# Performance work log

Measured on AMD Instinct MI355X. Metric: run time of the kernel, lower is better.

## Reference

```python
import jax, jax.numpy as jnp
import numpy as np

B = 2            # batch size
N_PRE = 50000    # presynaptic neurons
N_POST = 50000   # postsynaptic neurons
N_SYN = 10_000_000   # synapses (avg in-degree 200)
N_TYPES = 20     # synapse/receptor types (rows of basis table)
N_BASIS = 5      # receptor basis functions
SPIKE_P = 0.02   # spike probability per neuron per step


def setup_inputs() -> dict:
    key = jax.random.key(0)
    k1, k2, k3, k4, k5 = jax.random.split(key, 5)
    # binary spike buffer, like rec_z_buf (values in {0,1})
    rec_z_buf = (jax.random.uniform(k1, (B, N_PRE)) < SPIKE_P).astype(jnp.float32)
    weight_values = jax.random.normal(k2, (N_SYN,), dtype=jnp.float32) * 0.1
    synaptic_basis_weights = jax.random.uniform(k3, (N_TYPES, N_BASIS), dtype=jnp.float32)
    # col 0 = postsynaptic index, col 1 = presynaptic index
    synapse_indices = jax.random.randint(k4, (N_SYN, 2), 0, N_POST, dtype=jnp.int32)
    syn_ids = jax.random.randint(k5, (N_SYN,), 0, N_TYPES, dtype=jnp.int32)
    return {
        'rec_z_buf': rec_z_buf,
        'weight_values': weight_values,
        'synaptic_basis_weights': synaptic_basis_weights,
        'synapse_indices': synapse_indices,
        'syn_ids': syn_ids,
        'n_post': N_POST,
    }


def reference(rec_z_buf, weight_values, synaptic_basis_weights, synapse_indices, syn_ids, n_post):
    """I[b, post, r] = sum_syn spike[b, pre_syn] * W_syn * basis[syn_id_syn, r].

    Equivalent to the TF custom op: since spikes are binary, gating by
    spike > 0 equals multiplying by the spike value.
    Returns flat [B * n_post, n_basis] like i_rec_flat.
    """
    post = synapse_indices[:, 0]            # [n_syn]
    pre = synapse_indices[:, 1]             # [n_syn]
    # per-synapse weighted basis contribution [n_syn, R]
    contrib = weight_values[:, None] * synaptic_basis_weights[syn_ids]
    gathered = rec_z_buf[:, pre]            # [B, n_syn] spike gate per synapse
    per_syn = gathered[:, :, None] * contrib[None, :, :]   # [B, n_syn, R]
    # scatter-add into postsynaptic neurons, per batch element
    i_rec = jax.vmap(lambda x: jax.ops.segment_sum(x, post, num_segments=n_post))(per_syn)
    return i_rec.reshape(-1, i_rec.shape[-1])   # [B * n_post, R]
```

## Files before the change

### kernel.cpp

```cpp
#include <hip/hip_runtime.h>

#define N_PRE_C   50000
#define N_TYPES_C 20
#define N_BASIS_C 5
#define NB        2
#define WORDS32   1568

typedef unsigned long long ull;
typedef unsigned int uint_t;

__global__ __launch_bounds__(256) void pack_spikes(const float* __restrict__ rec_z,
                                                   uint_t* __restrict__ mask32,
                                                   float4* __restrict__ zbuf,
                                                   int zquads) {
    const int b = blockIdx.y;
    const int i = blockIdx.x * 256 + threadIdx.x;
    float v = 0.f;
    if (i < N_PRE_C) v = rec_z[b * N_PRE_C + i];
    const ull m = __ballot(v > 0.f);
    if ((threadIdx.x & 63) == 0) {
        const int w32 = i >> 5;
        mask32[(w32 + 0) * NB + b] = (uint_t)(m & 0xffffffffull);
        mask32[(w32 + 1) * NB + b] = (uint_t)(m >> 32);
    }

    if (zbuf != nullptr) {
        const int nt = gridDim.x * gridDim.y * 256;
        int q = (blockIdx.y * gridDim.x + blockIdx.x) * 256 + threadIdx.x;
        const float4 z = make_float4(0.f, 0.f, 0.f, 0.f);
        for (; q < zquads; q += nt) zbuf[q] = z;
    }
}

__global__ __launch_bounds__(256) void syn_scatter_t(
    const int4*  __restrict__ idx2,
    const float4* __restrict__ w4,
    const int4*  __restrict__ sid4,
    const uint2* __restrict__ mask2,
    float* __restrict__ out_t,
    int n_post, int n_syn) {
    __shared__ __align__(16) uint2 sm[WORDS32];
    {
        const uint4* msrc = (const uint4*)mask2;
        uint4* mdst = (uint4*)sm;
        for (int t = threadIdx.x; t < WORDS32 / 2; t += 256) mdst[t] = msrc[t];
    }
    __syncthreads();

    const int t = blockIdx.x * 256 + threadIdx.x;
    const long base = (long)t * 4;
    if (base >= n_syn) return;
    const int np20 = n_post * N_TYPES_C;

    if (base + 4 <= n_syn) {
        const int4 p01 = idx2[t * 2];
        const int4 p23 = idx2[t * 2 + 1];
        const uint2 m0 = sm[p01.y >> 5];
        const uint2 m1 = sm[p01.w >> 5];
        const uint2 m2 = sm[p23.y >> 5];
        const uint2 m3 = sm[p23.w >> 5];
        const uint_t b0 = 1u << (p01.y & 31);
        const uint_t b1 = 1u << (p01.w & 31);
        const uint_t b2 = 1u << (p23.y & 31);
        const uint_t b3 = 1u << (p23.w & 31);
        const uint_t f0 = (m0.x | m0.y) & b0;
        const uint_t f1 = (m1.x | m1.y) & b1;
        const uint_t f2 = (m2.x | m2.y) & b2;
        const uint_t f3 = (m3.x | m3.y) & b3;
        if (f0 | f1 | f2 | f3) {
            const float4 wv = w4[t];
            const int4   sv = sid4[t];
            if (f0) {
                const int o = p01.x * N_TYPES_C + sv.x;
                if (m0.x & b0) unsafeAtomicAdd(out_t + o, wv.x);
                if (m0.y & b0) unsafeAtomicAdd(out_t + o + np20, wv.x);
            }
            if (f1) {
                const int o = p01.z * N_TYPES_C + sv.y;
                if (m1.x & b1) unsafeAtomicAdd(out_t + o, wv.y);
                if (m1.y & b1) unsafeAtomicAdd(out_t + o + np20, wv.y);
            }
            if (f2) {
                const int o = p23.x * N_TYPES_C + sv.z;
                if (m2.x & b2) unsafeAtomicAdd(out_t + o, wv.z);
                if (m2.y & b2) unsafeAtomicAdd(out_t + o + np20, wv.z);
            }
            if (f3) {
                const int o = p23.z * N_TYPES_C + sv.w;
                if (m3.x & b3) unsafeAtomicAdd(out_t + o, wv.w);
                if (m3.y & b3) unsafeAtomicAdd(out_t + o + np20, wv.w);
            }
        }
    } else {
        const int*   idx = (const int*)idx2;
        const float* w   = (const float*)w4;
        const int*   sid = (const int*)sid4;
        for (long s = base; s < n_syn; ++s) {
            const int post = idx[2 * s], pre = idx[2 * s + 1];
            const uint2 mw = sm[pre >> 5];
            const uint_t bit = 1u << (pre & 31);
            if (((mw.x | mw.y) & bit) == 0u) continue;
            const int o = post * N_TYPES_C + sid[s];
            if (mw.x & bit) unsafeAtomicAdd(out_t + o, w[s]);
            if (mw.y & bit) unsafeAtomicAdd(out_t + o + np20, w[s]);
        }
    }
}

__global__ __launch_bounds__(256) void combine_basis(
    const float* __restrict__ out_t,
    const float* __restrict__ basis,
    float* __restrict__ out, int rows) {
    __shared__ float sb[N_TYPES_C * N_BASIS_C];
    if (threadIdx.x < N_TYPES_C * N_BASIS_C) sb[threadIdx.x] = basis[threadIdx.x];
    __syncthreads();

    const int r = blockIdx.x * 256 + threadIdx.x;
    if (r >= rows) return;
    const float4* p = (const float4*)(out_t + (long)r * N_TYPES_C);
    float4 v0 = p[0], v1 = p[1], v2 = p[2], v3 = p[3], v4 = p[4];
    float vt[N_TYPES_C] = {v0.x, v0.y, v0.z, v0.w, v1.x, v1.y, v1.z, v1.w,
                           v2.x, v2.y, v2.z, v2.w, v3.x, v3.y, v3.z, v3.w,
                           v4.x, v4.y, v4.z, v4.w};
    float acc[N_BASIS_C] = {0.f, 0.f, 0.f, 0.f, 0.f};
    #pragma unroll
    for (int t = 0; t < N_TYPES_C; ++t) {
        #pragma unroll
        for (int k = 0; k < N_BASIS_C; ++k)
            acc[k] += vt[t] * sb[t * N_BASIS_C + k];
    }
    float* o = out + (long)r * N_BASIS_C;
    #pragma unroll
    for (int k = 0; k < N_BASIS_C; ++k) o[k] = acc[k];
}

__global__ __launch_bounds__(256) void syn_scatter_direct(
    const int4* __restrict__ idx2, const float4* __restrict__ w4,
    const int4* __restrict__ sid4, const float* __restrict__ basis,
    const uint2* __restrict__ mask2, float* __restrict__ out,
    int n_post, int n_syn) {
    __shared__ __align__(16) uint2 sm[WORDS32];
    __shared__ float sb[N_TYPES_C][N_BASIS_C];
    for (int t = threadIdx.x; t < WORDS32; t += 256) sm[t] = mask2[t];
    for (int t = threadIdx.x; t < N_TYPES_C * N_BASIS_C; t += 256)
        ((float*)sb)[t] = basis[t];
    __syncthreads();
    const int t = blockIdx.x * 256 + threadIdx.x;
    const long base = (long)t * 4;
    if (base >= n_syn) return;

    auto apply = [&](int post, int pre, float wv, int tt) {
        const uint2 mw = sm[pre >> 5];
        const uint_t bit = 1u << (pre & 31);
        if (((mw.x | mw.y) & bit) == 0u) return;
        const float* bs = sb[tt];
        float c[N_BASIS_C];
        #pragma unroll
        for (int k = 0; k < N_BASIS_C; ++k) c[k] = wv * bs[k];
        if (mw.x & bit) {
            float* o = out + (long)post * N_BASIS_C;
            #pragma unroll
            for (int k = 0; k < N_BASIS_C; ++k) unsafeAtomicAdd(o + k, c[k]);
        }
        if (mw.y & bit) {
            float* o = out + (long)(n_post + post) * N_BASIS_C;
            #pragma unroll
            for (int k = 0; k < N_BASIS_C; ++k) unsafeAtomicAdd(o + k, c[k]);
        }
    };

    if (base + 4 <= n_syn) {
        const int4   p01 = idx2[t * 2];
        const int4   p23 = idx2[t * 2 + 1];
        const float4 wv  = w4[t];
        const int4   sv  = sid4[t];
        apply(p01.x, p01.y, wv.x, sv.x);
        apply(p01.z, p01.w, wv.y, sv.y);
        apply(p23.x, p23.y, wv.z, sv.z);
        apply(p23.z, p23.w, wv.w, sv.w);
    } else {
        const int*   idx = (const int*)idx2;
        const float* w   = (const float*)w4;
        const int*   sid = (const int*)sid4;
        for (long s = base; s < n_syn; ++s)
            apply(idx[2 * s], idx[2 * s + 1], w[s], sid[s]);
    }
}

extern "C" void kernel_launch(void* const* d_in, const int* in_sizes, int n_in,
                              void* d_out, int out_size, void* d_ws, size_t ws_size,
                              hipStream_t stream) {
    const float* rec_z   = (const float*)d_in[0];
    const float* weights = (const float*)d_in[1];
    const float* basis   = (const float*)d_in[2];
    const int*   synidx  = (const int*)d_in[3];
    const int*   synids  = (const int*)d_in[4];
    float*       out     = (float*)d_out;

    const int n_syn  = in_sizes[4];
    const int rows   = out_size / N_BASIS_C;
    const int n_post = rows / NB;
    const int n_thr  = (n_syn + 3) / 4;
    const int blocks = (n_thr + 255) / 256;

    const size_t out_t_bytes = (size_t)rows * N_TYPES_C * sizeof(float);
    const size_t mask_bytes  = (size_t)WORDS32 * NB * sizeof(uint_t);

    if (ws_size >= out_t_bytes + mask_bytes) {
        float*  out_t  = (float*)d_ws;
        uint_t* mask32 = (uint_t*)((char*)d_ws + out_t_bytes);

        const int zquads = (int)(out_t_bytes / sizeof(float4));
        pack_spikes<<<dim3(WORDS32 * 32 / 256, NB), 256, 0, stream>>>(
            rec_z, mask32, (float4*)out_t, zquads);

        syn_scatter_t<<<blocks, 256, 0, stream>>>(
            (const int4*)synidx, (const float4*)weights, (const int4*)synids,
            (const uint2*)mask32, out_t, n_post, n_syn);

        combine_basis<<<(rows + 255) / 256, 256, 0, stream>>>(out_t, basis, out, rows);
    } else {
        uint_t* mask32 = (uint_t*)d_ws;
        hipMemsetAsync(d_out, 0, (size_t)out_size * sizeof(float), stream);
        pack_spikes<<<dim3(WORDS32 * 32 / 256, NB), 256, 0, stream>>>(
            rec_z, mask32, nullptr, 0);
        syn_scatter_direct<<<blocks, 256, 0, stream>>>(
            (const int4*)synidx, (const float4*)weights, (const int4*)synids,
            basis, (const uint2*)mask32, out, n_post, n_syn);
    }
}
```

Before: 198.7 us.

## Fuse pack, scatter and basis combine into one cooperative persistent kernel

Replaces the three-kernel sequence (spike packing plus zeroing, synapse scatter, basis combine) with a single cooperative kernel that uses grid-wide syncs between phases and grid-stride loops sized to the occupancy limit, capped at 2048 blocks. It aims to remove kernel launch gaps and inter-kernel drain and tail overhead. In exchange it adds two grid barriers with fences, and far fewer resident threads to hide the latency of the gathers and atomics. It falls back to the old path if the cooperative launch fails.

```diff
diff --git a/kernel.cpp b/kernel.cpp
--- a/kernel.cpp
+++ b/kernel.cpp
@@ -1,13 +1,147 @@
 #include <hip/hip_runtime.h>
+#include <hip/hip_cooperative_groups.h>
+
+namespace cg = cooperative_groups;
 
 #define N_PRE_C   50000
 #define N_TYPES_C 20
 #define N_BASIS_C 5
 #define NB        2
 #define WORDS32   1568
+#define PACK_LANES (NB * WORDS32 * 32)
 
 typedef unsigned long long ull;
 typedef unsigned int uint_t;
+
+__global__ __launch_bounds__(256) void fused_all(
+    const float* __restrict__ rec_z,
+    const float4* __restrict__ w4,
+    const float* __restrict__ basis,
+    const int4*  __restrict__ idx2,
+    const int4*  __restrict__ sid4,
+    uint_t* __restrict__ mask32,
+    float*  __restrict__ out_t,
+    float*  __restrict__ out,
+    int n_post, int n_syn, int rows) {
+    __shared__ __align__(16) uint2 sm[WORDS32];
+    __shared__ float sb[N_TYPES_C * N_BASIS_C];
+
+    const int tid = threadIdx.x;
+    const int gid = blockIdx.x * 256 + tid;
+    const int nthreads = gridDim.x * 256;
+
+    if (tid < N_TYPES_C * N_BASIS_C) sb[tid] = basis[tid];
+
+    if (gid < PACK_LANES) {
+        const int b = gid / (WORDS32 * 32);
+        const int i = gid % (WORDS32 * 32);
+        float v = 0.f;
+        if (i < N_PRE_C) v = rec_z[b * N_PRE_C + i];
+        const ull m = __ballot(v > 0.f);
+        if ((tid & 63) == 0) {
+            const int w32 = i >> 5;
+            mask32[(w32 + 0) * NB + b] = (uint_t)(m & 0xffffffffull);
+            mask32[(w32 + 1) * NB + b] = (uint_t)(m >> 32);
+        }
+    }
+    {
+        const int zq = rows * N_TYPES_C / 4;
+        float4* zp = (float4*)out_t;
+        const float4 z = make_float4(0.f, 0.f, 0.f, 0.f);
+        for (int q = gid; q < zq; q += nthreads) zp[q] = z;
+    }
+
+    __threadfence();
+    cg::this_grid().sync();
+    __threadfence();
+
+    {
+        const uint4* msrc = (const uint4*)mask32;
+        uint4* mdst = (uint4*)sm;
+        for (int t = tid; t < WORDS32 / 2; t += 256) mdst[t] = msrc[t];
+    }
+    __syncthreads();
+
+    const int np20 = n_post * N_TYPES_C;
+    const int nq = n_syn >> 2;
+    for (int t = gid; t < nq; t += nthreads) {
+        const int4 p01 = idx2[(long)t * 2];
+        const int4 p23 = idx2[(long)t * 2 + 1];
+        const uint2 m0 = sm[p01.y >> 5];
+        const uint2 m1 = sm[p01.w >> 5];
+        const uint2 m2 = sm[p23.y >> 5];
+        const uint2 m3 = sm[p23.w >> 5];
+        const uint_t b0 = 1u << (p01.y & 31);
+        const uint_t b1 = 1u << (p01.w & 31);
+        const uint_t b2 = 1u << (p23.y & 31);
+        const uint_t b3 = 1u << (p23.w & 31);
+        const uint_t f0 = (m0.x | m0.y) & b0;
+        const uint_t f1 = (m1.x | m1.y) & b1;
+        const uint_t f2 = (m2.x | m2.y) & b2;
+        const uint_t f3 = (m3.x | m3.y) & b3;
+        if (f0 | f1 | f2 | f3) {
+            const float4 wv = w4[t];
+            const int4   sv = sid4[t];
+            if (f0) {
+                const int o = p01.x * N_TYPES_C + sv.x;
+                if (m0.x & b0) unsafeAtomicAdd(out_t + o, wv.x);
+                if (m0.y & b0) unsafeAtomicAdd(out_t + o + np20, wv.x);
+            }
+            if (f1) {
+                const int o = p01.z * N_TYPES_C + sv.y;
+                if (m1.x & b1) unsafeAtomicAdd(out_t + o, wv.y);
+                if (m1.y & b1) unsafeAtomicAdd(out_t + o + np20, wv.y);
+            }
+            if (f2) {
+                const int o = p23.x * N_TYPES_C + sv.z;
+                if (m2.x & b2) unsafeAtomicAdd(out_t + o, wv.z);
+                if (m2.y & b2) unsafeAtomicAdd(out_t + o + np20, wv.z);
+            }
+            if (f3) {
+                const int o = p23.z * N_TYPES_C + sv.w;
+                if (m3.x & b3) unsafeAtomicAdd(out_t + o, wv.w);
+                if (m3.y & b3) unsafeAtomicAdd(out_t + o + np20, wv.w);
+            }
+        }
+    }
+    const int rem = n_syn & 3;
+    if (blockIdx.x == 0 && tid < rem) {
+        const long s = (long)(n_syn & ~3) + tid;
+        const int*   idx = (const int*)idx2;
+        const float* w   = (const float*)w4;
+        const int*   sid = (const int*)sid4;
+        const int post = idx[2 * s], pre = idx[2 * s + 1];
+        const uint2 mw = sm[pre >> 5];
+        const uint_t bit = 1u << (pre & 31);
+        if ((mw.x | mw.y) & bit) {
+            const int o = post * N_TYPES_C + sid[s];
+            if (mw.x & bit) unsafeAtomicAdd(out_t + o, w[s]);
+            if (mw.y & bit) unsafeAtomicAdd(out_t + o + np20, w[s]);
+        }
+    }
+
+    __threadfence();
+    cg::this_grid().sync();
+    __threadfence();
+
+    for (int r = gid; r < rows; r += nthreads) {
+        const float4* p = (const float4*)(out_t + (long)r * N_TYPES_C);
+        float4 v0 = p[0], v1 = p[1], v2 = p[2], v3 = p[3], v4 = p[4];
+        float vt[N_TYPES_C] = {v0.x, v0.y, v0.z, v0.w, v1.x, v1.y, v1.z, v1.w,
+                               v2.x, v2.y, v2.z, v2.w, v3.x, v3.y, v3.z, v3.w,
+                               v4.x, v4.y, v4.z, v4.w};
+        float acc[N_BASIS_C] = {0.f, 0.f, 0.f, 0.f, 0.f};
+        #pragma unroll
+        for (int t = 0; t < N_TYPES_C; ++t) {
+            #pragma unroll
+            for (int k = 0; k < N_BASIS_C; ++k)
+                acc[k] += vt[t] * sb[t * N_BASIS_C + k];
+        }
+        float* o = out + (long)r * N_BASIS_C;
+        #pragma unroll
+        for (int k = 0; k < N_BASIS_C; ++k) o[k] = acc[k];
+    }
+}
 
 __global__ __launch_bounds__(256) void pack_spikes(const float* __restrict__ rec_z,
                                                    uint_t* __restrict__ mask32,
@@ -23,7 +157,6 @@
         mask32[(w32 + 0) * NB + b] = (uint_t)(m & 0xffffffffull);
         mask32[(w32 + 1) * NB + b] = (uint_t)(m >> 32);
     }
-
     if (zbuf != nullptr) {
         const int nt = gridDim.x * gridDim.y * 256;
         int q = (blockIdx.y * gridDim.x + blockIdx.x) * 256 + threadIdx.x;
@@ -46,12 +179,10 @@
         for (int t = threadIdx.x; t < WORDS32 / 2; t += 256) mdst[t] = msrc[t];
     }
     __syncthreads();
-
     const int t = blockIdx.x * 256 + threadIdx.x;
     const long base = (long)t * 4;
     if (base >= n_syn) return;
     const int np20 = n_post * N_TYPES_C;
-
     if (base + 4 <= n_syn) {
         const int4 p01 = idx2[t * 2];
         const int4 p23 = idx2[t * 2 + 1];
@@ -114,7 +245,6 @@
     __shared__ float sb[N_TYPES_C * N_BASIS_C];
     if (threadIdx.x < N_TYPES_C * N_BASIS_C) sb[threadIdx.x] = basis[threadIdx.x];
     __syncthreads();
-
     const int r = blockIdx.x * 256 + threadIdx.x;
     if (r >= rows) return;
     const float4* p = (const float4*)(out_t + (long)r * N_TYPES_C);
@@ -148,7 +278,6 @@
     const int t = blockIdx.x * 256 + threadIdx.x;
     const long base = (long)t * 4;
     if (base >= n_syn) return;
-
     auto apply = [&](int post, int pre, float wv, int tt) {
         const uint2 mw = sm[pre >> 5];
         const uint_t bit = 1u << (pre & 31);
@@ -168,7 +297,6 @@
             for (int k = 0; k < N_BASIS_C; ++k) unsafeAtomicAdd(o + k, c[k]);
         }
     };
-
     if (base + 4 <= n_syn) {
         const int4   p01 = idx2[t * 2];
         const int4   p23 = idx2[t * 2 + 1];
@@ -200,30 +328,58 @@
     const int n_syn  = in_sizes[4];
     const int rows   = out_size / N_BASIS_C;
     const int n_post = rows / NB;
-    const int n_thr  = (n_syn + 3) / 4;
-    const int blocks = (n_thr + 255) / 256;
 
     const size_t out_t_bytes = (size_t)rows * N_TYPES_C * sizeof(float);
     const size_t mask_bytes  = (size_t)WORDS32 * NB * sizeof(uint_t);
+
+    static int coop_blocks = -2;
+    if (coop_blocks == -2) {
+        int dev = 0, maxb = 0, ncu = 0;
+        if (hipGetDevice(&dev) == hipSuccess) {
+            hipDeviceProp_t prop;
+            if (hipGetDeviceProperties(&prop, dev) == hipSuccess)
+                ncu = prop.multiProcessorCount;
+            if (hipOccupancyMaxActiveBlocksPerMultiprocessor(
+                    &maxb, (const void*)fused_all, 256, 0) != hipSuccess)
+                maxb = 0;
+        }
+        long g = (long)maxb * ncu;
+        if (g > 2048) g = 2048;
+        coop_blocks = (g >= 256) ? (int)g : -1;
+    }
+
+    if (ws_size >= out_t_bytes + mask_bytes && coop_blocks > 0) {
+        float*  out_t  = (float*)d_ws;
+        uint_t* mask32 = (uint_t*)((char*)d_ws + out_t_bytes);
+
+        void* args[] = {(void*)&rec_z, (void*)&weights, (void*)&basis,
+                        (void*)&synidx, (void*)&synids, (void*)&mask32,
+                        (void*)&out_t, (void*)&out,
+                        (void*)&n_post, (void*)&n_syn, (void*)&rows};
+        const hipError_t e = hipLaunchCooperativeKernel(
+            (const void*)fused_all, dim3(coop_blocks), dim3(256),
+            args, 0, stream);
+        if (e == hipSuccess) return;
+        coop_blocks = -1;
+    }
 
     if (ws_size >= out_t_bytes + mask_bytes) {
         float*  out_t  = (float*)d_ws;
         uint_t* mask32 = (uint_t*)((char*)d_ws + out_t_bytes);
-
         const int zquads = (int)(out_t_bytes / sizeof(float4));
         pack_spikes<<<dim3(WORDS32 * 32 / 256, NB), 256, 0, stream>>>(
             rec_z, mask32, (float4*)out_t, zquads);
-
+        const int blocks = ((n_syn + 3) / 4 + 255) / 256;
         syn_scatter_t<<<blocks, 256, 0, stream>>>(
             (const int4*)synidx, (const float4*)weights, (const int4*)synids,
             (const uint2*)mask32, out_t, n_post, n_syn);
-
         combine_basis<<<(rows + 255) / 256, 256, 0, stream>>>(out_t, basis, out, rows);
     } else {
         uint_t* mask32 = (uint_t*)d_ws;
         hipMemsetAsync(d_out, 0, (size_t)out_size * sizeof(float), stream);
         pack_spikes<<<dim3(WORDS32 * 32 / 256, NB), 256, 0, stream>>>(
             rec_z, mask32, nullptr, 0);
+        const int blocks = ((n_syn + 3) / 4 + 255) / 256;
         syn_scatter_direct<<<blocks, 256, 0, stream>>>(
             (const int4*)synidx, (const float4*)weights, (const int4*)synids,
             basis, (const uint2*)mask32, out, n_post, n_syn);
```

New measurement: 482.7 us. +142.9%, slower.
